# Kernel optimization log

Measured on AMD Instinct MI355X. Metric: run time of the kernel, lower is better.

Reference implementation:

```python
import jax, jax.numpy as jnp
import numpy as np

N = 100000
D = 128
NEG_SLOPE = 0.2


def setup_inputs() -> dict:
    key = jax.random.key(0)
    ks = jax.random.split(key, 10)
    x = jax.random.normal(ks[0], (N, D), dtype=jnp.float32)
    edge_index = jax.random.randint(ks[1], (2, 625000), 0, N, dtype=jnp.int64)
    s = 1.0 / np.sqrt(D)
    W1 = jax.random.uniform(ks[2], (D, D), jnp.float32, -s, s)
    a_src1 = jax.random.uniform(ks[3], (D,), jnp.float32, -s, s)
    a_dst1 = jax.random.uniform(ks[4], (D,), jnp.float32, -s, s)
    b1 = jnp.zeros((D,), jnp.float32)
    W2 = jax.random.uniform(ks[5], (D, D), jnp.float32, -s, s)
    a_src2 = jax.random.uniform(ks[6], (D,), jnp.float32, -s, s)
    a_dst2 = jax.random.uniform(ks[7], (D,), jnp.float32, -s, s)
    b2 = jnp.zeros((D,), jnp.float32)
    return {"x": x, "edge_index": edge_index, "W1": W1, "a_src1": a_src1,
            "a_dst1": a_dst1, "b1": b1, "W2": W2, "a_src2": a_src2,
            "a_dst2": a_dst2, "b2": b2}


def _add_self_loops(edge_index, n):
    loops = jnp.arange(n, dtype=edge_index.dtype)
    return jnp.concatenate([edge_index, jnp.stack([loops, loops])], axis=1)


def _gat_conv(x, src, dst, W, a_src, a_dst, b, n):
    # Linear transform: [N, D]
    h = x @ W
    # Per-node attention logits, gathered onto edges (heads=1)
    e = jnp.take(h @ a_src, src) + jnp.take(h @ a_dst, dst)  # [E]
    e = jax.nn.leaky_relu(e, NEG_SLOPE)
    # Scatter-softmax over destination-node segments (every node has a self loop)
    m = jax.ops.segment_max(e, dst, num_segments=n)
    w = jnp.exp(e - jnp.take(m, dst))
    z = jax.ops.segment_sum(w, dst, num_segments=n)
    alpha = w / jnp.take(z, dst)  # [E]
    # Weighted scatter-add aggregate
    msg = alpha[:, None] * jnp.take(h, src, axis=0)  # [E, D]
    out = jax.ops.segment_sum(msg, dst, num_segments=n)
    return out + b


def reference(x, edge_index, W1, a_src1, a_dst1, b1, W2, a_src2, a_dst2, b2):
    n = x.shape[0]
    ei = _add_self_loops(edge_index, n)
    src, dst = ei[0], ei[1]
    h = jax.nn.relu(_gat_conv(x, src, dst, W1, a_src1, a_dst1, b1, n))
    h = jax.nn.relu(_gat_conv(h, src, dst, W2, a_src2, a_dst2, b2, n))
    return h
```

## Files before the change

kernel.cpp:

```cpp
#include <hip/hip_runtime.h>

#define D 128
#define WS (D + 8)
#define NEG_SLOPE 0.2f
#define SLOTS 20
#define OVF_CAP 4096

using v8f16 = __attribute__((ext_vector_type(8))) _Float16;
using v2h   = __attribute__((ext_vector_type(2))) _Float16;
using f32x4 = __attribute__((ext_vector_type(4))) float;


__global__ __launch_bounds__(256) void prep_kernel(const float* __restrict__ W1,
        const float* __restrict__ W2, _Float16* __restrict__ Wt1,
        _Float16* __restrict__ Wt2, int* __restrict__ cnt, int* __restrict__ csr,
        int* __restrict__ ovf_n, int n) {
    int t = blockIdx.x * 256 + threadIdx.x;
    if (t == 0) *ovf_n = 0;
    for (int i = t; i < n; i += 32768) {
        cnt[i] = 0;
        #pragma unroll
        for (int j = 0; j < 8; ++j) csr[i * SLOTS + j] = i;
    }
    int which = t >> 14;
    int idx = t & 16383;
    int k = idx & (D - 1);
    int c = idx >> 7;
    const float* W = which ? W2 : W1;
    _Float16* Wt = which ? Wt2 : Wt1;
    Wt[(size_t)c * D + k] = (_Float16)W[(size_t)k * D + c];
}


template<bool F16IN>
__device__ __forceinline__ void gemm_body(int bid, const void* __restrict__ Xv,
        const _Float16* __restrict__ Wt, const float* __restrict__ a_src,
        const float* __restrict__ a_dst, _Float16* __restrict__ H,
        float* __restrict__ hs, float* __restrict__ hd, int n,
        _Float16* wl) {
    const int lane = threadIdx.x & 63;
    const int wave = threadIdx.x >> 6;
    const int gl = lane & 15;
    const int q = lane >> 4;
    const int row0 = bid * 128 + wave * 16;

    int arow = row0 + gl;
    if (arow >= n) arow = n - 1;

    v8f16 afr[4];
    #pragma unroll
    for (int kc = 0; kc < 4; ++kc) {
        if constexpr (F16IN) {
            const _Float16* Xh = (const _Float16*)Xv;
            afr[kc] = *(const v8f16*)&Xh[(size_t)arow * D + kc * 32 + q * 8];
        } else {
            const float* p = &((const float*)Xv)[(size_t)arow * D + kc * 32 + q * 8];
            float4 x0 = *(const float4*)p;
            float4 x1 = *(const float4*)(p + 4);
            v8f16 t;
            t[0] = (_Float16)x0.x; t[1] = (_Float16)x0.y;
            t[2] = (_Float16)x0.z; t[3] = (_Float16)x0.w;
            t[4] = (_Float16)x1.x; t[5] = (_Float16)x1.y;
            t[6] = (_Float16)x1.z; t[7] = (_Float16)x1.w;
            afr[kc] = t;
        }
    }

    for (int i = threadIdx.x; i < D * D / 8; i += 512) {
        int r = i >> 4;
        int c = (i & 15) * 8;
        *(v8f16*)&wl[r * WS + c] = *(const v8f16*)&Wt[r * D + c];
    }
    __syncthreads();

    f32x4 acc[8];
    #pragma unroll
    for (int t = 0; t < 8; ++t) acc[t] = (f32x4){0.f, 0.f, 0.f, 0.f};

    #pragma unroll
    for (int kc = 0; kc < 4; ++kc) {
        #pragma unroll
        for (int t = 0; t < 8; ++t) {
            v8f16 bfr = *(const v8f16*)&wl[(t * 16 + gl) * WS + kc * 32 + q * 8];
            acc[t] = __builtin_amdgcn_mfma_f32_16x16x32_f16(afr[kc], bfr, acc[t], 0, 0, 0);
        }
    }

    float asv[8], adv[8];
    #pragma unroll
    for (int t = 0; t < 8; ++t) { asv[t] = a_src[t * 16 + gl]; adv[t] = a_dst[t * 16 + gl]; }

    #pragma unroll
    for (int r = 0; r < 4; ++r) {
        int row = row0 + q * 4 + r;
        bool ok = row < n;
        float ps = 0.f, pd = 0.f;
        #pragma unroll
        for (int t = 0; t < 8; ++t) {
            float v = acc[t][r];
            ps = fmaf(v, asv[t], ps);
            pd = fmaf(v, adv[t], pd);
            if (ok) H[(size_t)row * D + t * 16 + gl] = (_Float16)v;
        }
        #pragma unroll
        for (int dlt = 8; dlt > 0; dlt >>= 1) {
            ps += __shfl_down(ps, dlt, 16);
            pd += __shfl_down(pd, dlt, 16);
        }
        if (ok && gl == 0) { hs[row] = ps; hd[row] = pd; }
    }
}


__global__ __launch_bounds__(512) void mega1_kernel(
        const float* __restrict__ x, const _Float16* __restrict__ Wt1,
        const float* __restrict__ a_src1, const float* __restrict__ a_dst1,
        _Float16* __restrict__ h, float* __restrict__ hs, float* __restrict__ hd,
        const int* __restrict__ ei, int* __restrict__ cnt, int* __restrict__ csr,
        int* __restrict__ ovf_n, int* __restrict__ ovf,
        int gb, int e_in, int n) {
    __shared__ _Float16 wl[D * WS];
    int b = blockIdx.x;
    int rid;
    if (b < 2 * gb) {
        if ((b & 1) == 0) {
            gemm_body<false>(b >> 1, x, Wt1, a_src1, a_dst1, h, hs, hd, n, wl);
            return;
        }
        rid = b >> 1;
    } else {
        rid = b - gb;
    }
    int e = rid * 512 + threadIdx.x;
    int tot = e_in + n;
    if (e >= tot) return;
    int s, d;
    if (e < e_in) { s = ei[e]; d = ei[e_in + e]; }
    else          { s = e - e_in; d = s; }
    int r = atomicAdd(&cnt[d], 1);
    if (r < SLOTS) {
        csr[d * SLOTS + r] = s;
    } else {
        int ix = atomicAdd(ovf_n, 1);
        if (ix < OVF_CAP) { ovf[2 * ix] = d; ovf[2 * ix + 1] = s; }
    }
}

__global__ __launch_bounds__(512) void gemm2_kernel(
        const _Float16* __restrict__ tb, const _Float16* __restrict__ Wt2,
        const float* __restrict__ a_src2, const float* __restrict__ a_dst2,
        _Float16* __restrict__ h, float* __restrict__ hs, float* __restrict__ hd,
        int n) {
    __shared__ _Float16 wl[D * WS];
    gemm_body<true>(blockIdx.x, tb, Wt2, a_src2, a_dst2, h, hs, hd, n, wl);
}


__device__ __forceinline__ v2h pack_lo(uint a, uint b) {
    v2h r;
    r.x = __builtin_bit_cast(_Float16, (unsigned short)(a & 0xffffu));
    r.y = __builtin_bit_cast(_Float16, (unsigned short)(b & 0xffffu));
    return r;
}
__device__ __forceinline__ v2h pack_hi(uint a, uint b) {
    v2h r;
    r.x = __builtin_bit_cast(_Float16, (unsigned short)(a >> 16));
    r.y = __builtin_bit_cast(_Float16, (unsigned short)(b >> 16));
    return r;
}
__device__ __forceinline__ float lo_f(uint a) {
    return (float)__builtin_bit_cast(_Float16, (unsigned short)(a & 0xffffu));
}
__device__ __forceinline__ float hi_f(uint a) {
    return (float)__builtin_bit_cast(_Float16, (unsigned short)(a >> 16));
}

__device__ __forceinline__ void acc_pair(float* acc, const uint4& rA,
        const uint4& rB, float w0, float w1) {
#if __has_builtin(__builtin_amdgcn_fdot2)
    v2h wp; wp.x = (_Float16)w0; wp.y = (_Float16)w1;
    acc[0] = __builtin_amdgcn_fdot2(pack_lo(rA.x, rB.x), wp, acc[0], false);
    acc[1] = __builtin_amdgcn_fdot2(pack_hi(rA.x, rB.x), wp, acc[1], false);
    acc[2] = __builtin_amdgcn_fdot2(pack_lo(rA.y, rB.y), wp, acc[2], false);
    acc[3] = __builtin_amdgcn_fdot2(pack_hi(rA.y, rB.y), wp, acc[3], false);
    acc[4] = __builtin_amdgcn_fdot2(pack_lo(rA.z, rB.z), wp, acc[4], false);
    acc[5] = __builtin_amdgcn_fdot2(pack_hi(rA.z, rB.z), wp, acc[5], false);
    acc[6] = __builtin_amdgcn_fdot2(pack_lo(rA.w, rB.w), wp, acc[6], false);
    acc[7] = __builtin_amdgcn_fdot2(pack_hi(rA.w, rB.w), wp, acc[7], false);
#else
    acc[0] = fmaf(w0, lo_f(rA.x), acc[0]); acc[1] = fmaf(w0, hi_f(rA.x), acc[1]);
    acc[2] = fmaf(w0, lo_f(rA.y), acc[2]); acc[3] = fmaf(w0, hi_f(rA.y), acc[3]);
    acc[4] = fmaf(w0, lo_f(rA.z), acc[4]); acc[5] = fmaf(w0, hi_f(rA.z), acc[5]);
    acc[6] = fmaf(w0, lo_f(rA.w), acc[6]); acc[7] = fmaf(w0, hi_f(rA.w), acc[7]);
    acc[0] = fmaf(w1, lo_f(rB.x), acc[0]); acc[1] = fmaf(w1, hi_f(rB.x), acc[1]);
    acc[2] = fmaf(w1, lo_f(rB.y), acc[2]); acc[3] = fmaf(w1, hi_f(rB.y), acc[3]);
    acc[4] = fmaf(w1, lo_f(rB.z), acc[4]); acc[5] = fmaf(w1, hi_f(rB.z), acc[5]);
    acc[6] = fmaf(w1, lo_f(rB.w), acc[6]); acc[7] = fmaf(w1, hi_f(rB.w), acc[7]);
#endif
}

template<bool OUT_F16>
__global__ __launch_bounds__(256) void aggregate_kernel(
        const _Float16* __restrict__ h, const float* __restrict__ hs,
        const float* __restrict__ hd, const int* __restrict__ cnt,
        const int* __restrict__ csr, const int* __restrict__ ovf_n,
        const int* __restrict__ ovf, const float* __restrict__ bias,
        float* __restrict__ outf, _Float16* __restrict__ outb, int n) {
    int nodeA = (blockIdx.x * 4 + (threadIdx.x >> 6)) * 2;
    if (nodeA >= n) return;
    int nodeB = nodeA + 1;
    bool hasB = nodeB < n;
    int nBs = hasB ? nodeB : nodeA;
    int lane = threadIdx.x & 63;
    int grp = lane >> 4;
    int gl = lane & 15;
    const int baseA = nodeA * SLOTS;
    const int baseB = nBs * SLOTS;
    const uint* hp = (const uint*)h;

    int degA = cnt[nodeA];
    int degB = cnt[nBs];
    float hdA = hd[nodeA];
    float hdB = hd[nBs];
    int jb = grp * 2;
    int cA0 = csr[baseA + jb];
    int cA1 = csr[baseA + jb + 1];
    int cB0 = csr[baseB + jb];
    int cB1 = csr[baseB + jb + 1];
    int sA0 = ((uint)cA0 < (uint)n) ? cA0 : nodeA;
    int sA1 = ((uint)cA1 < (uint)n) ? cA1 : nodeA;
    int sB0 = ((uint)cB0 < (uint)n) ? cB0 : nBs;
    int sB1 = ((uint)cB1 < (uint)n) ? cB1 : nBs;
    uint4 rA0 = *(const uint4*)(hp + ((size_t)sA0 << 6) + (gl << 2));
    uint4 rA1 = *(const uint4*)(hp + ((size_t)sA1 << 6) + (gl << 2));
    uint4 rB0 = *(const uint4*)(hp + ((size_t)sB0 << 6) + (gl << 2));
    uint4 rB1 = *(const uint4*)(hp + ((size_t)sB1 << 6) + (gl << 2));
    float eA0 = hs[sA0] + hdA;
    float eA1 = hs[sA1] + hdA;
    float eB0 = hs[sB0] + hdB;
    float eB1 = hs[sB1] + hdB;

    float accA[8] = {0.f, 0.f, 0.f, 0.f, 0.f, 0.f, 0.f, 0.f};
    float accB[8] = {0.f, 0.f, 0.f, 0.f, 0.f, 0.f, 0.f, 0.f};
    float zA = 0.f, zB = 0.f;

    int mindA = degA < SLOTS ? degA : SLOTS;
    int mindB = degB < SLOTS ? degB : SLOTS;
    eA0 = eA0 > 0.f ? eA0 : NEG_SLOPE * eA0;
    eA1 = eA1 > 0.f ? eA1 : NEG_SLOPE * eA1;
    eB0 = eB0 > 0.f ? eB0 : NEG_SLOPE * eB0;
    eB1 = eB1 > 0.f ? eB1 : NEG_SLOPE * eB1;
    float wA0 = (jb < mindA) ? __expf(eA0) : 0.f;
    float wA1 = (jb + 1 < mindA) ? __expf(eA1) : 0.f;
    float wB0 = (jb < mindB) ? __expf(eB0) : 0.f;
    float wB1 = (jb + 1 < mindB) ? __expf(eB1) : 0.f;
    zA += wA0 + wA1;
    zB += wB0 + wB1;
    acc_pair(accA, rA0, rA1, wA0, wA1);
    acc_pair(accB, rB0, rB1, wB0, wB1);

    int ntA = (mindA + 7) >> 3;
    for (int u = 1; u < ntA; ++u) {
        int i0 = u * 8 + jb;
        bool a0 = i0 < mindA;
        bool a1 = i0 + 1 < mindA;
        int t0 = a0 ? csr[baseA + i0] : nodeA;
        int t1 = a1 ? csr[baseA + i0 + 1] : nodeA;
        uint4 qA = *(const uint4*)(hp + ((size_t)t0 << 6) + (gl << 2));
        uint4 qB = *(const uint4*)(hp + ((size_t)t1 << 6) + (gl << 2));
        float f0 = hs[t0] + hdA;
        f0 = f0 > 0.f ? f0 : NEG_SLOPE * f0;
        float f1 = hs[t1] + hdA;
        f1 = f1 > 0.f ? f1 : NEG_SLOPE * f1;
        float v0 = a0 ? __expf(f0) : 0.f;
        float v1 = a1 ? __expf(f1) : 0.f;
        zA += v0 + v1;
        acc_pair(accA, qA, qB, v0, v1);
    }
    int ntB = (mindB + 7) >> 3;
    for (int u = 1; u < ntB; ++u) {
        int i0 = u * 8 + jb;
        bool a0 = i0 < mindB;
        bool a1 = i0 + 1 < mindB;
        int t0 = a0 ? csr[baseB + i0] : nBs;
        int t1 = a1 ? csr[baseB + i0 + 1] : nBs;
        uint4 qA = *(const uint4*)(hp + ((size_t)t0 << 6) + (gl << 2));
        uint4 qB = *(const uint4*)(hp + ((size_t)t1 << 6) + (gl << 2));
        float f0 = hs[t0] + hdB;
        f0 = f0 > 0.f ? f0 : NEG_SLOPE * f0;
        float f1 = hs[t1] + hdB;
        f1 = f1 > 0.f ? f1 : NEG_SLOPE * f1;
        float v0 = a0 ? __expf(f0) : 0.f;
        float v1 = a1 ? __expf(f1) : 0.f;
        zB += v0 + v1;
        acc_pair(accB, qA, qB, v0, v1);
    }

    if (degA > SLOTS || degB > SLOTS) {
        int m = *ovf_n;
        if (m > OVF_CAP) m = OVF_CAP;
        for (int i = 0; i < m; ++i) {
            int od = ovf[2 * i];
            if (od == nodeA || (hasB && od == nodeB)) {
                bool isA = (od == nodeA);
                int os = ovf[2 * i + 1];
                float e = hs[os] + (isA ? hdA : hdB);
                e = e > 0.f ? e : NEG_SLOPE * e;
                float wv = __expf(e);
                if (grp == 0) {
                    uint4 rr = *(const uint4*)(hp + ((size_t)os << 6) + (gl << 2));
                    float* ac = isA ? accA : accB;
                    ac[0] = fmaf(wv, lo_f(rr.x), ac[0]); ac[1] = fmaf(wv, hi_f(rr.x), ac[1]);
                    ac[2] = fmaf(wv, lo_f(rr.y), ac[2]); ac[3] = fmaf(wv, hi_f(rr.y), ac[3]);
                    ac[4] = fmaf(wv, lo_f(rr.z), ac[4]); ac[5] = fmaf(wv, hi_f(rr.z), ac[5]);
                    ac[6] = fmaf(wv, lo_f(rr.w), ac[6]); ac[7] = fmaf(wv, hi_f(rr.w), ac[7]);
                    if (isA) zA += wv; else zB += wv;
                }
            }
        }
    }

    #pragma unroll
    for (int dlt = 32; dlt >= 16; dlt >>= 1) {
        #pragma unroll
        for (int k = 0; k < 8; ++k) {
            accA[k] += __shfl_down(accA[k], dlt, 64);
            accB[k] += __shfl_down(accB[k], dlt, 64);
        }
        zA += __shfl_down(zA, dlt, 64);
        zB += __shfl_down(zB, dlt, 64);
    }
    if (lane < 16) {
        float4 b0 = *(const float4*)&bias[lane * 8];
        float4 b1 = *(const float4*)&bias[lane * 8 + 4];
        float invA = 1.0f / zA;
        float oA[8];
        oA[0] = accA[0] * invA + b0.x; oA[1] = accA[1] * invA + b0.y;
        oA[2] = accA[2] * invA + b0.z; oA[3] = accA[3] * invA + b0.w;
        oA[4] = accA[4] * invA + b1.x; oA[5] = accA[5] * invA + b1.y;
        oA[6] = accA[6] * invA + b1.z; oA[7] = accA[7] * invA + b1.w;
        #pragma unroll
        for (int k = 0; k < 8; ++k) oA[k] = oA[k] > 0.f ? oA[k] : 0.f;
        if constexpr (OUT_F16) {
            alignas(16) _Float16 ob[8];
            #pragma unroll
            for (int k = 0; k < 8; ++k) ob[k] = (_Float16)oA[k];
            *(uint4*)&outb[(size_t)nodeA * D + lane * 8] = *(const uint4*)ob;
        } else {
            float* op = outf + (size_t)nodeA * D + lane * 8;
            *(float4*)op = make_float4(oA[0], oA[1], oA[2], oA[3]);
            *(float4*)(op + 4) = make_float4(oA[4], oA[5], oA[6], oA[7]);
        }
        if (hasB) {
            float invB = 1.0f / zB;
            float oB[8];
            oB[0] = accB[0] * invB + b0.x; oB[1] = accB[1] * invB + b0.y;
            oB[2] = accB[2] * invB + b0.z; oB[3] = accB[3] * invB + b0.w;
            oB[4] = accB[4] * invB + b1.x; oB[5] = accB[5] * invB + b1.y;
            oB[6] = accB[6] * invB + b1.z; oB[7] = accB[7] * invB + b1.w;
            #pragma unroll
            for (int k = 0; k < 8; ++k) oB[k] = oB[k] > 0.f ? oB[k] : 0.f;
            if constexpr (OUT_F16) {
                alignas(16) _Float16 ob[8];
                #pragma unroll
                for (int k = 0; k < 8; ++k) ob[k] = (_Float16)oB[k];
                *(uint4*)&outb[(size_t)nodeB * D + lane * 8] = *(const uint4*)ob;
            } else {
                float* op = outf + (size_t)nodeB * D + lane * 8;
                *(float4*)op = make_float4(oB[0], oB[1], oB[2], oB[3]);
                *(float4*)(op + 4) = make_float4(oB[4], oB[5], oB[6], oB[7]);
            }
        }
    }
}


extern "C" void kernel_launch(void* const* d_in, const int* in_sizes, int n_in,
                              void* d_out, int out_size, void* d_ws, size_t ws_size,
                              hipStream_t stream) {
    const float* x      = (const float*)d_in[0];
    const int*   ei     = (const int*)d_in[1];
    const float* W1     = (const float*)d_in[2];
    const float* a_src1 = (const float*)d_in[3];
    const float* a_dst1 = (const float*)d_in[4];
    const float* b1     = (const float*)d_in[5];
    const float* W2     = (const float*)d_in[6];
    const float* a_src2 = (const float*)d_in[7];
    const float* a_dst2 = (const float*)d_in[8];
    const float* b2     = (const float*)d_in[9];

    int n    = in_sizes[0] / D;
    int e_in = in_sizes[1] / 2;
    int e_tot = e_in + n;

    _Float16* h   = (_Float16*)d_ws;
    _Float16* Wt1 = h + (size_t)n * D;
    _Float16* Wt2 = Wt1 + D * D;
    float* hs     = (float*)(Wt2 + D * D);
    float* hd     = hs + n;
    int*   cnt    = (int*)(hd + n);
    int*   ovf_n  = cnt + n;
    int*   ovf    = ovf_n + 1;
    int*   csr    = ovf + 2 * OVF_CAP;
    _Float16* tb  = (_Float16*)d_out;

    int eb = (e_tot + 511) / 512;
    int nb8 = (n + 7) / 8;
    int gb = (n + 127) / 128;

    prep_kernel<<<128, 256, 0, stream>>>(W1, W2, Wt1, Wt2, cnt, csr, ovf_n, n);
    mega1_kernel<<<gb + eb, 512, 0, stream>>>(x, Wt1, a_src1, a_dst1, h, hs, hd,
                                              ei, cnt, csr, ovf_n, ovf, gb, e_in, n);
    aggregate_kernel<true><<<nb8, 256, 0, stream>>>(h, hs, hd, cnt, csr, ovf_n, ovf,
                                                    b1, nullptr, tb, n);
    gemm2_kernel<<<gb, 512, 0, stream>>>(tb, Wt2, a_src2, a_dst2, h, hs, hd, n);
    aggregate_kernel<false><<<nb8, 256, 0, stream>>>(h, hs, hd, cnt, csr, ovf_n, ovf,
                                                     b2, (float*)d_out, nullptr, n);
}
```

Measured before the change: 229.2 us.

## Stage weights via direct global-to-LDS XOR-swizzled loads and batch edge scatter

Replaces the padded LDS copy of the transposed weight with an XOR-swizzled unpadded layout, filled through global_load_lds direct-to-LDS transfers when the builtin is available. B-fragment reads use the matching swizzle to avoid bank conflicts. The edge-bucketing blocks now process two edges per thread, halving their count, and the interleaving of GEMM and scatter blocks is re-balanced around the edge block count. This aims to cut LDS staging cost, register traffic and block count, but the two-edge path adds per-thread work and reorders scheduling.

Result: slower. 234.2 us (+2.2%).

```diff
diff --git a/kernel.cpp b/kernel.cpp
--- a/kernel.cpp
+++ b/kernel.cpp
@@ -1,7 +1,6 @@
 #include <hip/hip_runtime.h>
 
 #define D 128
-#define WS (D + 8)
 #define NEG_SLOPE 0.2f
 #define SLOTS 20
 #define OVF_CAP 4096
@@ -31,6 +30,29 @@
     Wt[(size_t)c * D + k] = (_Float16)W[(size_t)k * D + c];
 }
 
+
+
+__device__ __forceinline__ void stage_w(const _Float16* __restrict__ Wt,
+                                        _Float16* wl) {
+    const int tid = threadIdx.x;
+    #pragma unroll
+    for (int k = 0; k < 4; ++k) {
+        int i = k * 512 + tid;
+        int r = i >> 4;
+        int sb = ((i & 15) * 16) ^ ((r & 7) << 4);
+#if __has_builtin(__builtin_amdgcn_global_load_lds)
+        __builtin_amdgcn_global_load_lds(
+            (const __attribute__((address_space(1))) unsigned int*)
+                ((const char*)Wt + (size_t)r * 256 + sb),
+            (__attribute__((address_space(3))) unsigned int*)
+                ((char*)wl + (size_t)i * 16),
+            16, 0, 0);
+#else
+        *(v8f16*)((char*)wl + (size_t)i * 16) =
+            *(const v8f16*)((const char*)Wt + (size_t)r * 256 + sb);
+#endif
+    }
+}
 
 template<bool F16IN>
 __device__ __forceinline__ void gemm_body(int bid, const void* __restrict__ Xv,
@@ -66,22 +88,20 @@
         }
     }
 
-    for (int i = threadIdx.x; i < D * D / 8; i += 512) {
-        int r = i >> 4;
-        int c = (i & 15) * 8;
-        *(v8f16*)&wl[r * WS + c] = *(const v8f16*)&Wt[r * D + c];
-    }
+    stage_w(Wt, wl);
     __syncthreads();
 
     f32x4 acc[8];
     #pragma unroll
     for (int t = 0; t < 8; ++t) acc[t] = (f32x4){0.f, 0.f, 0.f, 0.f};
 
+    const int xr = (gl & 7) << 4;
     #pragma unroll
     for (int kc = 0; kc < 4; ++kc) {
         #pragma unroll
         for (int t = 0; t < 8; ++t) {
-            v8f16 bfr = *(const v8f16*)&wl[(t * 16 + gl) * WS + kc * 32 + q * 8];
+            v8f16 bfr = *(const v8f16*)((const char*)wl +
+                    (size_t)(t * 16 + gl) * 256 + ((kc * 64 + q * 16) ^ xr));
             acc[t] = __builtin_amdgcn_mfma_f32_16x16x32_f16(afr[kc], bfr, acc[t], 0, 0, 0);
         }
     }
@@ -118,31 +138,48 @@
         _Float16* __restrict__ h, float* __restrict__ hs, float* __restrict__ hd,
         const int* __restrict__ ei, int* __restrict__ cnt, int* __restrict__ csr,
         int* __restrict__ ovf_n, int* __restrict__ ovf,
-        int gb, int e_in, int n) {
-    __shared__ _Float16 wl[D * WS];
+        int eb, int e_in, int n) {
+    __shared__ _Float16 wl[D * D];
     int b = blockIdx.x;
     int rid;
-    if (b < 2 * gb) {
+    if (b < 2 * eb) {
         if ((b & 1) == 0) {
             gemm_body<false>(b >> 1, x, Wt1, a_src1, a_dst1, h, hs, hd, n, wl);
             return;
         }
         rid = b >> 1;
     } else {
-        rid = b - gb;
-    }
-    int e = rid * 512 + threadIdx.x;
+        gemm_body<false>(b - eb, x, Wt1, a_src1, a_dst1, h, hs, hd, n, wl);
+        return;
+    }
     int tot = e_in + n;
-    if (e >= tot) return;
-    int s, d;
-    if (e < e_in) { s = ei[e]; d = ei[e_in + e]; }
-    else          { s = e - e_in; d = s; }
-    int r = atomicAdd(&cnt[d], 1);
-    if (r < SLOTS) {
-        csr[d * SLOTS + r] = s;
-    } else {
-        int ix = atomicAdd(ovf_n, 1);
-        if (ix < OVF_CAP) { ovf[2 * ix] = d; ovf[2 * ix + 1] = s; }
+    int e0 = rid * 1024 + threadIdx.x;
+    int e1 = e0 + 512;
+    bool v0 = e0 < tot, v1 = e1 < tot;
+    int s0 = 0, d0 = 0, s1 = 0, d1 = 0;
+    if (v0) {
+        if (e0 < e_in) { s0 = ei[e0]; d0 = ei[e_in + e0]; }
+        else           { s0 = e0 - e_in; d0 = s0; }
+    }
+    if (v1) {
+        if (e1 < e_in) { s1 = ei[e1]; d1 = ei[e_in + e1]; }
+        else           { s1 = e1 - e_in; d1 = s1; }
+    }
+    int r0 = v0 ? atomicAdd(&cnt[d0], 1) : 0;
+    int r1 = v1 ? atomicAdd(&cnt[d1], 1) : 0;
+    if (v0) {
+        if (r0 < SLOTS) csr[d0 * SLOTS + r0] = s0;
+        else {
+            int ix = atomicAdd(ovf_n, 1);
+            if (ix < OVF_CAP) { ovf[2 * ix] = d0; ovf[2 * ix + 1] = s0; }
+        }
+    }
+    if (v1) {
+        if (r1 < SLOTS) csr[d1 * SLOTS + r1] = s1;
+        else {
+            int ix = atomicAdd(ovf_n, 1);
+            if (ix < OVF_CAP) { ovf[2 * ix] = d1; ovf[2 * ix + 1] = s1; }
+        }
     }
 }
 
@@ -151,7 +188,7 @@
         const float* __restrict__ a_src2, const float* __restrict__ a_dst2,
         _Float16* __restrict__ h, float* __restrict__ hs, float* __restrict__ hd,
         int n) {
-    __shared__ _Float16 wl[D * WS];
+    __shared__ _Float16 wl[D * D];
     gemm_body<true>(blockIdx.x, tb, Wt2, a_src2, a_dst2, h, hs, hd, n, wl);
 }
 
@@ -404,13 +441,13 @@
     int*   csr    = ovf + 2 * OVF_CAP;
     _Float16* tb  = (_Float16*)d_out;
 
-    int eb = (e_tot + 511) / 512;
+    int eb = (e_tot + 1023) / 1024;
     int nb8 = (n + 7) / 8;
     int gb = (n + 127) / 128;
 
     prep_kernel<<<128, 256, 0, stream>>>(W1, W2, Wt1, Wt2, cnt, csr, ovf_n, n);
     mega1_kernel<<<gb + eb, 512, 0, stream>>>(x, Wt1, a_src1, a_dst1, h, hs, hd,
-                                              ei, cnt, csr, ovf_n, ovf, gb, e_in, n);
+                                              ei, cnt, csr, ovf_n, ovf, eb, e_in, n);
     aggregate_kernel<true><<<nb8, 256, 0, stream>>>(h, hs, hd, cnt, csr, ovf_n, ovf,
                                                     b1, nullptr, tb, n);
     gemm2_kernel<<<gb, 512, 0, stream>>>(tb, Wt2, a_src2, a_dst2, h, hs, hd, n);
```
